# Performance work log

Measured on AMD Instinct MI355X. Metric: run time of the kernel, lower is better.

Reference implementation:

```python
import jax, jax.numpy as jnp
import numpy as np

NUM_GRAPHS = 2048  # graph.batch_size
EPS = 1e-6


def setup_inputs() -> dict:
    key = jax.random.key(0)
    k1, k2 = jax.random.split(key)
    N, D = 1000000, 128
    feat = jax.random.normal(k1, (N, D), dtype=jnp.float32)
    segment_ids = jnp.sort(jax.random.randint(k2, (N,), 0, NUM_GRAPHS)).astype(jnp.int64)
    weight = jnp.ones((D,), dtype=jnp.float32)
    bias = jnp.zeros((D,), dtype=jnp.float32)
    mean_scale = jnp.ones((D,), dtype=jnp.float32)
    return {"feat": feat, "segment_ids": segment_ids, "weight": weight,
            "bias": bias, "mean_scale": mean_scale}


def reference(feat, segment_ids, weight, bias, mean_scale):
    # counts per graph ( == graph.batch_num_nodes() ). Clamp to 1 so that
    # empty segments (which never contribute to the output) don't produce NaNs.
    counts = jnp.maximum(
        jax.ops.segment_sum(jnp.ones_like(segment_ids, dtype=feat.dtype),
                            segment_ids, num_segments=NUM_GRAPHS), 1.0)
    inv_counts = (1.0 / counts)[:, None]                      # [B, 1]

    # per-graph mean: scatter_add then divide by segment size
    mean = jax.ops.segment_sum(feat, segment_ids, num_segments=NUM_GRAPHS) * inv_counts  # [B, D]
    sub = feat - mean[segment_ids] * mean_scale               # [N, D]

    # per-graph std of the mean-shifted features
    var = jax.ops.segment_sum(sub * sub, segment_ids, num_segments=NUM_GRAPHS) * inv_counts
    std = jnp.sqrt(var + EPS)                                 # [B, D]

    return weight * sub / std[segment_ids] + bias
```

## Files before the change

### kernel.cpp

```cpp
#include <hip/hip_runtime.h>

#define D 128
#define NSEG 2048
#define EPSV 1e-6f
#define BLOCK 512
#define CPR 32
#define RG (BLOCK/CPR)
#define WAVES (BLOCK/64)
#define MAXK 32

typedef float f32x4 __attribute__((ext_vector_type(4)));

__global__ __launch_bounds__(BLOCK, 2) void graphnorm_fused(
    const float* __restrict__ feat,
    const int* __restrict__ seg,
    const float* __restrict__ weight,
    const float* __restrict__ bias,
    const float* __restrict__ mean_scale,
    float* __restrict__ out,
    int N)
{
    const int s = blockIdx.x;
    __shared__ int s_range[2];
    __shared__ f32x4 s_sum[WAVES][CPR];
    __shared__ f32x4 s_sq[WAVES][CPR];
    __shared__ f32x4 s_a[CPR];
    __shared__ f32x4 s_b[CPR];

    const int t = threadIdx.x;

    if (t < 2) {
        int target = s + t;
        int lo = 0, hi = N;
        while (lo < hi) {
            int mid = (lo + hi) >> 1;
            if (seg[mid] < target) lo = mid + 1; else hi = mid;
        }
        s_range[t] = lo;
    }
    __syncthreads();
    const int start = s_range[0];
    const int end   = s_range[1];

    const int c = t & (CPR - 1);
    const int g = t >> 5;

    const f32x4* feat4 = reinterpret_cast<const f32x4*>(feat);
    f32x4* out4 = reinterpret_cast<f32x4*>(out);

    f32x4 buf[MAXK];
    #pragma unroll
    for (int k = 0; k < MAXK; ++k) {
        const int r = start + g + k * RG;
        if (r < end) buf[k] = feat4[r * CPR + c];
    }

    f32x4 s0 = 0.f, q0 = 0.f;
    #pragma unroll
    for (int k = 0; k < MAXK; ++k) {
        const int r = start + g + k * RG;
        if (r < end) {
            s0 += buf[k];
            q0 += buf[k] * buf[k];
        }
    }

    const int tail_base = start + g + MAXK * RG;
    for (int r = tail_base; r < end; r += RG) {
        f32x4 v = feat4[r * CPR + c];
        s0 += v;
        q0 += v * v;
    }

    #pragma unroll
    for (int i = 0; i < 4; ++i) {
        s0[i] += __shfl_xor(s0[i], 32);
        q0[i] += __shfl_xor(q0[i], 32);
    }

    const int w    = t >> 6;
    const int lane = t & 63;
    if (lane < 32) {
        s_sum[w][c] = s0;
        s_sq[w][c]  = q0;
    }
    __syncthreads();

    if (t < CPR) {
        f32x4 sm = s_sum[0][t];
        f32x4 sg = s_sq[0][t];
        #pragma unroll
        for (int i = 1; i < WAVES; ++i) {
            sm += s_sum[i][t];
            sg += s_sq[i][t];
        }
        const float cnt = (float)max(end - start, 1);
        const float inv = 1.0f / cnt;
        const f32x4 wv  = reinterpret_cast<const f32x4*>(weight)[t];
        const f32x4 bi  = reinterpret_cast<const f32x4*>(bias)[t];
        const f32x4 msc = reinterpret_cast<const f32x4*>(mean_scale)[t];
        f32x4 A, B;
        #pragma unroll
        for (int i = 0; i < 4; ++i) {
            float mean = sm[i] * inv;
            float ms   = mean * msc[i];
            float var  = fmaxf(sg[i] * inv - 2.f * mean * ms + ms * ms, 0.f);
            float istd = rsqrtf(var + EPSV);
            A[i] = wv[i] * istd;
            B[i] = bi[i] - A[i] * ms;
        }
        s_a[t] = A;
        s_b[t] = B;
    }
    __syncthreads();

    const f32x4 A = s_a[c];
    const f32x4 B = s_b[c];

    #pragma unroll
    for (int k = 0; k < MAXK; ++k) {
        const int r = start + g + k * RG;
        if (r < end)
            __builtin_nontemporal_store(A * buf[k] + B, &out4[r * CPR + c]);
    }
    for (int r = tail_base; r < end; r += RG) {
        f32x4 v = feat4[r * CPR + c];
        __builtin_nontemporal_store(A * v + B, &out4[r * CPR + c]);
    }
}

extern "C" void kernel_launch(void* const* d_in, const int* in_sizes, int n_in,
                              void* d_out, int out_size, void* d_ws, size_t ws_size,
                              hipStream_t stream) {
    const float* feat       = (const float*)d_in[0];
    const int*   seg        = (const int*)d_in[1];
    const float* weight     = (const float*)d_in[2];
    const float* bias       = (const float*)d_in[3];
    const float* mean_scale = (const float*)d_in[4];
    float* out = (float*)d_out;

    const int N = in_sizes[0] / D;

    graphnorm_fused<<<NSEG, BLOCK, 0, stream>>>(
        feat, seg, weight, bias, mean_scale, out, N);
}
```

Baseline: 227.5 us.

## Split each segment across four blocks by feature column quarter

```diff
diff --git a/kernel.cpp b/kernel.cpp
--- a/kernel.cpp
+++ b/kernel.cpp
@@ -3,15 +3,16 @@
 #define D 128
 #define NSEG 2048
 #define EPSV 1e-6f
-#define BLOCK 512
-#define CPR 32
-#define RG (BLOCK/CPR)
+#define BLOCK 256
+#define QCH 8
+#define CPRF 32
+#define RG (BLOCK/QCH)
 #define WAVES (BLOCK/64)
-#define MAXK 32
+#define MAXK 16
 
 typedef float f32x4 __attribute__((ext_vector_type(4)));
 
-__global__ __launch_bounds__(BLOCK, 2) void graphnorm_fused(
+__global__ __launch_bounds__(BLOCK, 4) void graphnorm_fused(
     const float* __restrict__ feat,
     const int* __restrict__ seg,
     const float* __restrict__ weight,
@@ -20,12 +21,14 @@
     float* __restrict__ out,
     int N)
 {
-    const int s = blockIdx.x;
+    const int bid = blockIdx.x;
+    const int s = bid >> 2;
+    const int q = bid & 3;
     __shared__ int s_range[2];
-    __shared__ f32x4 s_sum[WAVES][CPR];
-    __shared__ f32x4 s_sq[WAVES][CPR];
-    __shared__ f32x4 s_a[CPR];
-    __shared__ f32x4 s_b[CPR];
+    __shared__ f32x4 s_sum[WAVES][QCH];
+    __shared__ f32x4 s_sq[WAVES][QCH];
+    __shared__ f32x4 s_a[QCH];
+    __shared__ f32x4 s_b[QCH];
 
     const int t = threadIdx.x;
 
@@ -42,8 +45,9 @@
     const int start = s_range[0];
     const int end   = s_range[1];
 
-    const int c = t & (CPR - 1);
-    const int g = t >> 5;
+    const int c = t & (QCH - 1);
+    const int g = t >> 3;
+    const int chunk = q * QCH + c;
 
     const f32x4* feat4 = reinterpret_cast<const f32x4*>(feat);
     f32x4* out4 = reinterpret_cast<f32x4*>(out);
@@ -52,7 +56,7 @@
     #pragma unroll
     for (int k = 0; k < MAXK; ++k) {
         const int r = start + g + k * RG;
-        if (r < end) buf[k] = feat4[r * CPR + c];
+        if (r < end) buf[k] = feat4[r * CPRF + chunk];
     }
 
     f32x4 s0 = 0.f, q0 = 0.f;
@@ -67,26 +71,30 @@
 
     const int tail_base = start + g + MAXK * RG;
     for (int r = tail_base; r < end; r += RG) {
-        f32x4 v = feat4[r * CPR + c];
+        f32x4 v = feat4[r * CPRF + chunk];
         s0 += v;
         q0 += v * v;
     }
 
     #pragma unroll
     for (int i = 0; i < 4; ++i) {
+        s0[i] += __shfl_xor(s0[i], 8);
+        s0[i] += __shfl_xor(s0[i], 16);
         s0[i] += __shfl_xor(s0[i], 32);
+        q0[i] += __shfl_xor(q0[i], 8);
+        q0[i] += __shfl_xor(q0[i], 16);
         q0[i] += __shfl_xor(q0[i], 32);
     }
 
     const int w    = t >> 6;
     const int lane = t & 63;
-    if (lane < 32) {
-        s_sum[w][c] = s0;
-        s_sq[w][c]  = q0;
+    if (lane < QCH) {
+        s_sum[w][lane] = s0;
+        s_sq[w][lane]  = q0;
     }
     __syncthreads();
 
-    if (t < CPR) {
+    if (t < QCH) {
         f32x4 sm = s_sum[0][t];
         f32x4 sg = s_sq[0][t];
         #pragma unroll
@@ -96,9 +104,10 @@
         }
         const float cnt = (float)max(end - start, 1);
         const float inv = 1.0f / cnt;
-        const f32x4 wv  = reinterpret_cast<const f32x4*>(weight)[t];
-        const f32x4 bi  = reinterpret_cast<const f32x4*>(bias)[t];
-        const f32x4 msc = reinterpret_cast<const f32x4*>(mean_scale)[t];
+        const int wc = q * QCH + t;
+        const f32x4 wv  = reinterpret_cast<const f32x4*>(weight)[wc];
+        const f32x4 bi  = reinterpret_cast<const f32x4*>(bias)[wc];
+        const f32x4 msc = reinterpret_cast<const f32x4*>(mean_scale)[wc];
         f32x4 A, B;
         #pragma unroll
         for (int i = 0; i < 4; ++i) {
@@ -121,11 +130,11 @@
     for (int k = 0; k < MAXK; ++k) {
         const int r = start + g + k * RG;
         if (r < end)
-            __builtin_nontemporal_store(A * buf[k] + B, &out4[r * CPR + c]);
+            __builtin_nontemporal_store(A * buf[k] + B, &out4[r * CPRF + chunk]);
     }
     for (int r = tail_base; r < end; r += RG) {
-        f32x4 v = feat4[r * CPR + c];
-        __builtin_nontemporal_store(A * v + B, &out4[r * CPR + c]);
+        f32x4 v = feat4[r * CPRF + chunk];
+        __builtin_nontemporal_store(A * v + B, &out4[r * CPRF + chunk]);
     }
 }
 
@@ -141,6 +150,6 @@
 
     const int N = in_sizes[0] / D;
 
-    graphnorm_fused<<<NSEG, BLOCK, 0, stream>>>(
+    graphnorm_fused<<<NSEG * 4, BLOCK, 0, stream>>>(
         feat, seg, weight, bias, mean_scale, out, N);
 }
```

Result: faster. 200.9 us (median of 2 runs) (-11.7%).
